# Kernel tuning notes

Hardware: AMD Instinct MI355X
Metric: run time of the kernel (lower is better)

## Reference

```python
import jax, jax.numpy as jnp
import numpy as np

EPS = 1e-5


def _conv(x, w, padding, groups=1):
    return jax.lax.conv_general_dilated(
        x, w, window_strides=(1, 1),
        padding=[(padding, padding), (padding, padding)],
        dimension_numbers=("NCHW", "OIHW", "NCHW"),
        feature_group_count=groups)


def _bn(x, gamma, beta, mean, var):
    # inference-mode BatchNorm2d, params shape [C]
    inv = gamma * jax.lax.rsqrt(var + EPS)
    return x * inv[None, :, None, None] + (beta - mean * inv)[None, :, None, None]


def _adder_dw(x, w):
    # depthwise AdderNet 'conv': out[b, c*R+r, h, w] = -sum_{kh,kw} |x[b,c,h+kh-p,w+kw-p] - w[c,r,kh,kw]|
    # x: [B,C,H,W], w: [C,R,K,K] (groups=C, R outputs per group)
    B, C, H, W = x.shape
    R, K = w.shape[1], w.shape[-1]
    p = K // 2
    xp = jnp.pad(x, ((0, 0), (0, 0), (p, p), (p, p)))
    acc = jnp.zeros((B, C, R, H, W), x.dtype)
    for kh in range(K):          # fixed small 3x3 tap loop
        for kw in range(K):
            shift = xp[:, :, kh:kh + H, kw:kw + W]          # [B,C,H,W]
            tap = w[:, :, kh, kw]                           # [C,R]
            acc = acc + jnp.abs(shift[:, :, None] - tap[None, :, :, None, None])
    return -acc.reshape(B, C * R, H, W)


def setup_inputs() -> dict:
    key = jax.random.key(0)
    ks = jax.random.split(key, 12)
    B, Cin, H, W = 32, 240, 56, 56
    init_c, ratio = 24, 10
    r1 = ratio - 1            # 9 ghost channels per primary channel
    new_c = init_c * r1       # 216
    f32 = jnp.float32
    x = jax.random.normal(ks[0], (B, Cin, H, W), f32)
    w_primary = jax.random.normal(ks[1], (init_c, Cin, 1, 1), f32) * 0.05
    w_dw = jax.random.normal(ks[2], (init_c, 1, 3, 3), f32) * 0.1
    w_add = jax.random.normal(ks[3], (init_c, r1, 3, 3), f32) * 0.1
    def bn(kk, c):
        k1, k2 = jax.random.split(kk)
        return (jnp.ones((c,), f32), jnp.zeros((c,), f32),
                jax.random.normal(k1, (c,), f32) * 0.1,
                jax.random.uniform(k2, (c,), f32, 0.5, 1.5))
    g1, b1, m1, v1 = bn(ks[4], init_c)
    g2, b2, m2, v2 = bn(ks[5], init_c)
    g3, b3, m3, v3 = bn(ks[6], new_c)
    return dict(x=x, w_primary=w_primary, g1=g1, b1=b1, m1=m1, v1=v1,
                w_dw=w_dw, g2=g2, b2=b2, m2=m2, v2=v2,
                w_add=w_add, g3=g3, b3=b3, m3=m3, v3=v3)


def reference(x, w_primary, g1, b1, m1, v1, w_dw, g2, b2, m2, v2,
              w_add, g3, b3, m3, v3):
    oup = 240
    init_c = w_primary.shape[0]
    # primary_conv: 1x1 conv -> BN -> depthwise 3x3 conv -> BN -> Identity (relu slot is Identity)
    x1 = _conv(x, w_primary, padding=0)
    x1 = _bn(x1, g1, b1, m1, v1)
    x1 = _conv(x1, w_dw, padding=1, groups=init_c)
    x1 = _bn(x1, g2, b2, m2, v2)
    # cheap_operation: depthwise Adder2D -> BN -> ReLU
    x2 = _adder_dw(x1, w_add)
    x2 = jax.nn.relu(_bn(x2, g3, b3, m3, v3))
    out = jnp.concatenate([x1, x2], axis=1)
    return out[:, :oup]
```

## Files before the change

kernel.cpp:

```cpp
#include <hip/hip_runtime.h>

#define EPS_ 1e-5f
#define BATCH 32
#define CIN 240
#define H_ 56
#define W_ 56
#define HW 3136
#define C1 24
#define R_ 9
#define C2 216
#define COUT 240

#define WS_WT   0
#define WS_B1   5760
#define WS_WDW  5784
#define WS_B2   6000
#define WS_INV3 6024
#define WS_T3   6240

__global__ __launch_bounds__(256) void prep_kernel(
    const float* __restrict__ wp,
    const float* __restrict__ g1, const float* __restrict__ b1,
    const float* __restrict__ m1, const float* __restrict__ v1,
    const float* __restrict__ wdw,
    const float* __restrict__ g2, const float* __restrict__ b2,
    const float* __restrict__ m2, const float* __restrict__ v2,
    const float* __restrict__ g3, const float* __restrict__ b3,
    const float* __restrict__ m3, const float* __restrict__ v3,
    float* __restrict__ ws) {
  int i = blockIdx.x * 256 + threadIdx.x;
  if (i < 5760) {
    int ci = i / C1, co = i % C1;
    float s = g1[co] / sqrtf(v1[co] + EPS_);
    ws[WS_WT + ci * C1 + co] = wp[co * CIN + ci] * s;
    if (ci == 0) ws[WS_B1 + co] = b1[co] - m1[co] * s;
  } else if (i < 5760 + C2) {
    int j = i - 5760;
    int c = j / 9;
    float s = g2[c] / sqrtf(v2[c] + EPS_);
    ws[WS_WDW + j] = wdw[j] * s;
    if (j % 9 == 0) ws[WS_B2 + c] = b2[c] - m2[c] * s;
  } else if (i < 5976 + C2) {
    int j = i - 5976;
    float s = g3[j] / sqrtf(v3[j] + EPS_);
    ws[WS_INV3 + j] = s;
    ws[WS_T3 + j] = b3[j] - m3[j] * s;
  }
}

__global__ __launch_bounds__(256) void conv1x1_kernel(
    const float* __restrict__ x, const float* __restrict__ wt,
    const float* __restrict__ bias1, float* __restrict__ out) {
  __shared__ float smem[6144];
  const int tid  = threadIdx.x;
  const int lane = tid & 63;
  const int kq   = tid >> 6;

  for (int i = tid; i < 5760; i += 256) smem[i] = wt[i];
  __syncthreads();

  const int P   = blockIdx.x * 64 + lane;
  const int b   = P / HW;
  const int hw  = P - b * HW;
  const int ci0 = kq * 60;
  const float* xp    = x + ((size_t)b * CIN + ci0) * HW + hw;
  const float* wbase = smem + ci0 * C1;

  float acc[C1];
#pragma unroll
  for (int i = 0; i < C1; ++i) acc[i] = 0.f;

  float A[6], B[6];
#pragma unroll
  for (int j = 0; j < 6; ++j) A[j] = xp[(size_t)j * HW];
#pragma unroll
  for (int j = 0; j < 6; ++j) B[j] = xp[(size_t)(6 + j) * HW];

  auto consume = [&](const float* buf, int cb) {
#pragma unroll
    for (int j = 0; j < 6; ++j) {
      const float xv = buf[j];
      const float* wr = wbase + (cb + j) * C1;
#pragma unroll
      for (int k = 0; k < 6; ++k) {
        const float4 wq = *(const float4*)(wr + 4 * k);
        acc[4*k+0] = fmaf(wq.x, xv, acc[4*k+0]);
        acc[4*k+1] = fmaf(wq.y, xv, acc[4*k+1]);
        acc[4*k+2] = fmaf(wq.z, xv, acc[4*k+2]);
        acc[4*k+3] = fmaf(wq.w, xv, acc[4*k+3]);
      }
    }
  };

#pragma unroll 1
  for (int g = 0; g < 4; ++g) {
    const int c = 12 * g;
    consume(A, c);
#pragma unroll
    for (int j = 0; j < 6; ++j) A[j] = xp[(size_t)(c + 12 + j) * HW];
    consume(B, c + 6);
#pragma unroll
    for (int j = 0; j < 6; ++j) B[j] = xp[(size_t)(c + 18 + j) * HW];
  }
  consume(A, 48);
  consume(B, 54);
  __syncthreads();

#pragma unroll
  for (int i = 0; i < C1; ++i) smem[(kq * C1 + i) * 64 + lane] = acc[i];
  __syncthreads();

  float* o = out + ((size_t)b * COUT + C1) * HW + hw;
#pragma unroll
  for (int i = 0; i < 6; ++i) {
    const int co = kq * 6 + i;
    float v = smem[(0 * C1 + co) * 64 + lane]
            + smem[(1 * C1 + co) * 64 + lane]
            + smem[(2 * C1 + co) * 64 + lane]
            + smem[(3 * C1 + co) * 64 + lane]
            + bias1[co];
    o[(size_t)co * HW] = v;
  }
}

__global__ __launch_bounds__(256) void dw_kernel(
    const float* __restrict__ outr, const float* __restrict__ wdwf,
    const float* __restrict__ bias2, float* __restrict__ out) {
  const int c = blockIdx.y, b = blockIdx.z;
  const int q = blockIdx.x * 256 + threadIdx.x;
  if (q >= 784) return;
  const int h  = q / 14;
  const int w0 = (q - h * 14) * 4;
  const float* in = outr + ((size_t)b * COUT + C1 + c) * HW;

  float wk[9];
#pragma unroll
  for (int k = 0; k < 9; ++k) wk[k] = wdwf[c * 9 + k];
  const float bb = bias2[c];

  float xr[3][6];
#pragma unroll
  for (int kh = 0; kh < 3; ++kh) {
    const int hh = h + kh - 1;
    const bool rok = (hh >= 0) & (hh < H_);
    const float* rp = in + hh * W_;
    xr[kh][0] = (rok && w0 > 0) ? rp[w0 - 1] : 0.f;
    if (rok) {
      const float4 m = *(const float4*)(rp + w0);
      xr[kh][1] = m.x; xr[kh][2] = m.y; xr[kh][3] = m.z; xr[kh][4] = m.w;
    } else {
      xr[kh][1] = 0.f; xr[kh][2] = 0.f; xr[kh][3] = 0.f; xr[kh][4] = 0.f;
    }
    xr[kh][5] = (rok && w0 < W_ - 4) ? rp[w0 + 4] : 0.f;
  }

  float4 v = {bb, bb, bb, bb};
#pragma unroll
  for (int kh = 0; kh < 3; ++kh) {
#pragma unroll
    for (int kw = 0; kw < 3; ++kw) {
      const float t = wk[kh * 3 + kw];
      v.x = fmaf(xr[kh][kw + 0], t, v.x);
      v.y = fmaf(xr[kh][kw + 1], t, v.y);
      v.z = fmaf(xr[kh][kw + 2], t, v.z);
      v.w = fmaf(xr[kh][kw + 3], t, v.w);
    }
  }
  *(float4*)(out + ((size_t)b * COUT + c) * HW + h * W_ + w0) = v;
}

__global__ __launch_bounds__(256) void adder_kernel(
    const float* __restrict__ outr, const float* __restrict__ wadd,
    const float* __restrict__ inv3, const float* __restrict__ t3,
    float* __restrict__ out) {
  const int c = blockIdx.y, b = blockIdx.z;
  __shared__ float taps[R_][3][4];
  __shared__ float s3[R_], t3s[R_];
  const int tid = threadIdx.x;
  if (tid < 108) {
    int r = tid / 12, kh = (tid / 4) % 3, kw = tid & 3;
    taps[r][kh][kw] = (kw < 3) ? wadd[((c * R_ + r) * 3 + kh) * 3 + kw] : 0.f;
  } else if (tid >= 128 && tid < 128 + R_) {
    int r = tid - 128;
    s3[r]  = inv3[c * R_ + r];
    t3s[r] = t3[c * R_ + r];
  }
  __syncthreads();

  const int q = blockIdx.x * 256 + tid;
  if (q >= 784) return;
  const int h  = q / 14;
  const int w0 = (q - h * 14) * 4;
  const float* in = outr + ((size_t)b * COUT + c) * HW;

  float xr[3][6];
#pragma unroll
  for (int kh = 0; kh < 3; ++kh) {
    const int hh = h + kh - 1;
    const bool rok = (hh >= 0) & (hh < H_);
    const float* rp = in + hh * W_;
    xr[kh][0] = (rok && w0 > 0) ? rp[w0 - 1] : 0.f;
    if (rok) {
      const float4 m = *(const float4*)(rp + w0);
      xr[kh][1] = m.x; xr[kh][2] = m.y; xr[kh][3] = m.z; xr[kh][4] = m.w;
    } else {
      xr[kh][1] = 0.f; xr[kh][2] = 0.f; xr[kh][3] = 0.f; xr[kh][4] = 0.f;
    }
    xr[kh][5] = (rok && w0 < W_ - 4) ? rp[w0 + 4] : 0.f;
  }

#pragma unroll
  for (int r = 0; r < R_; ++r) {
    float a0 = 0.f, a1 = 0.f, a2 = 0.f, a3 = 0.f;
#pragma unroll
    for (int kh = 0; kh < 3; ++kh) {
#pragma unroll
      for (int kw = 0; kw < 3; ++kw) {
        const float t = taps[r][kh][kw];
        a0 += fabsf(xr[kh][kw + 0] - t);
        a1 += fabsf(xr[kh][kw + 1] - t);
        a2 += fabsf(xr[kh][kw + 2] - t);
        a3 += fabsf(xr[kh][kw + 3] - t);
      }
    }
    const float s = s3[r], bb = t3s[r];
    float4 v;
    v.x = fmaxf(fmaf(-s, a0, bb), 0.f);
    v.y = fmaxf(fmaf(-s, a1, bb), 0.f);
    v.z = fmaxf(fmaf(-s, a2, bb), 0.f);
    v.w = fmaxf(fmaf(-s, a3, bb), 0.f);
    *(float4*)(out + ((size_t)b * COUT + C1 + c * R_ + r) * HW + h * W_ + w0) = v;
  }
}

extern "C" void kernel_launch(void* const* d_in, const int* in_sizes, int n_in,
                              void* d_out, int out_size, void* d_ws, size_t ws_size,
                              hipStream_t stream) {
  const float* x    = (const float*)d_in[0];
  const float* wp   = (const float*)d_in[1];
  const float* g1   = (const float*)d_in[2];
  const float* b1   = (const float*)d_in[3];
  const float* m1   = (const float*)d_in[4];
  const float* v1   = (const float*)d_in[5];
  const float* wdw  = (const float*)d_in[6];
  const float* g2   = (const float*)d_in[7];
  const float* b2   = (const float*)d_in[8];
  const float* m2   = (const float*)d_in[9];
  const float* v2   = (const float*)d_in[10];
  const float* wadd = (const float*)d_in[11];
  const float* g3   = (const float*)d_in[12];
  const float* b3   = (const float*)d_in[13];
  const float* m3   = (const float*)d_in[14];
  const float* v3   = (const float*)d_in[15];

  float* ws  = (float*)d_ws;
  float* out = (float*)d_out;

  prep_kernel<<<25, 256, 0, stream>>>(wp, g1, b1, m1, v1, wdw, g2, b2, m2, v2,
                                      g3, b3, m3, v3, ws);

  conv1x1_kernel<<<1568, 256, 0, stream>>>(x, ws + WS_WT, ws + WS_B1, out);

  dw_kernel<<<dim3(4, C1, BATCH), 256, 0, stream>>>(out, ws + WS_WDW,
                                                    ws + WS_B2, out);

  adder_kernel<<<dim3(4, C1, BATCH), 256, 0, stream>>>(out, wadd, ws + WS_INV3,
                                                       ws + WS_T3, out);
}
```

Measured before the change: 220.6 us.

## Fuse depthwise conv and adder into one tiled kernel; widen conv1x1 per thread

Fuses the depthwise 3x3 conv and the depthwise adder into one kernel. Each block stages a row tile of the 1x1 conv output in shared memory, computes the x1 tile with a halo, and then computes the nine adder outputs from shared memory. This removes one launch and the global round trip of x1. The 1x1 conv now computes two pixels per thread with float2 loads and writes into a workspace buffer, so it uses half as many blocks and twice the accumulator registers. A fallback to the old three-kernel path is used when the workspace is too small.

```diff
diff --git a/kernel.cpp b/kernel.cpp
--- a/kernel.cpp
+++ b/kernel.cpp
@@ -17,6 +17,8 @@
 #define WS_B2   6000
 #define WS_INV3 6024
 #define WS_T3   6240
+#define WS_T1   8192
+#define WS_T1_FLOATS (8192 + BATCH * C1 * HW)
 
 __global__ __launch_bounds__(256) void prep_kernel(
     const float* __restrict__ wp,
@@ -50,8 +52,9 @@
 
 __global__ __launch_bounds__(256) void conv1x1_kernel(
     const float* __restrict__ x, const float* __restrict__ wt,
-    const float* __restrict__ bias1, float* __restrict__ out) {
-  __shared__ float smem[6144];
+    const float* __restrict__ bias1, float* __restrict__ t1b,
+    const int cs, const int coff) {
+  __shared__ float smem[12288];
   const int tid  = threadIdx.x;
   const int lane = tid & 63;
   const int kq   = tid >> 6;
@@ -59,35 +62,39 @@
   for (int i = tid; i < 5760; i += 256) smem[i] = wt[i];
   __syncthreads();
 
-  const int P   = blockIdx.x * 64 + lane;
+  const int P   = blockIdx.x * 128 + lane * 2;
   const int b   = P / HW;
   const int hw  = P - b * HW;
   const int ci0 = kq * 60;
   const float* xp    = x + ((size_t)b * CIN + ci0) * HW + hw;
   const float* wbase = smem + ci0 * C1;
 
-  float acc[C1];
-#pragma unroll
-  for (int i = 0; i < C1; ++i) acc[i] = 0.f;
-
-  float A[6], B[6];
-#pragma unroll
-  for (int j = 0; j < 6; ++j) A[j] = xp[(size_t)j * HW];
-#pragma unroll
-  for (int j = 0; j < 6; ++j) B[j] = xp[(size_t)(6 + j) * HW];
-
-  auto consume = [&](const float* buf, int cb) {
+  float acc[C1][2];
+#pragma unroll
+  for (int i = 0; i < C1; ++i) { acc[i][0] = 0.f; acc[i][1] = 0.f; }
+
+  float2 A[6], B[6];
+#pragma unroll
+  for (int j = 0; j < 6; ++j) A[j] = *(const float2*)(xp + (size_t)j * HW);
+#pragma unroll
+  for (int j = 0; j < 6; ++j) B[j] = *(const float2*)(xp + (size_t)(6 + j) * HW);
+
+  auto consume = [&](const float2* buf, int cb) {
 #pragma unroll
     for (int j = 0; j < 6; ++j) {
-      const float xv = buf[j];
+      const float2 xv = buf[j];
       const float* wr = wbase + (cb + j) * C1;
 #pragma unroll
       for (int k = 0; k < 6; ++k) {
         const float4 wq = *(const float4*)(wr + 4 * k);
-        acc[4*k+0] = fmaf(wq.x, xv, acc[4*k+0]);
-        acc[4*k+1] = fmaf(wq.y, xv, acc[4*k+1]);
-        acc[4*k+2] = fmaf(wq.z, xv, acc[4*k+2]);
-        acc[4*k+3] = fmaf(wq.w, xv, acc[4*k+3]);
+        acc[4*k+0][0] = fmaf(wq.x, xv.x, acc[4*k+0][0]);
+        acc[4*k+0][1] = fmaf(wq.x, xv.y, acc[4*k+0][1]);
+        acc[4*k+1][0] = fmaf(wq.y, xv.x, acc[4*k+1][0]);
+        acc[4*k+1][1] = fmaf(wq.y, xv.y, acc[4*k+1][1]);
+        acc[4*k+2][0] = fmaf(wq.z, xv.x, acc[4*k+2][0]);
+        acc[4*k+2][1] = fmaf(wq.z, xv.y, acc[4*k+2][1]);
+        acc[4*k+3][0] = fmaf(wq.w, xv.x, acc[4*k+3][0]);
+        acc[4*k+3][1] = fmaf(wq.w, xv.y, acc[4*k+3][1]);
       }
     }
   };
@@ -97,31 +104,136 @@
     const int c = 12 * g;
     consume(A, c);
 #pragma unroll
-    for (int j = 0; j < 6; ++j) A[j] = xp[(size_t)(c + 12 + j) * HW];
+    for (int j = 0; j < 6; ++j) A[j] = *(const float2*)(xp + (size_t)(c + 12 + j) * HW);
     consume(B, c + 6);
 #pragma unroll
-    for (int j = 0; j < 6; ++j) B[j] = xp[(size_t)(c + 18 + j) * HW];
+    for (int j = 0; j < 6; ++j) B[j] = *(const float2*)(xp + (size_t)(c + 18 + j) * HW);
   }
   consume(A, 48);
   consume(B, 54);
   __syncthreads();
 
 #pragma unroll
-  for (int i = 0; i < C1; ++i) smem[(kq * C1 + i) * 64 + lane] = acc[i];
-  __syncthreads();
-
-  float* o = out + ((size_t)b * COUT + C1) * HW + hw;
+  for (int i = 0; i < C1; ++i)
+    *(float2*)&smem[(kq * C1 + i) * 128 + 2 * lane] = make_float2(acc[i][0], acc[i][1]);
+  __syncthreads();
+
+  float* o = t1b + ((size_t)b * cs + coff) * HW + hw;
 #pragma unroll
   for (int i = 0; i < 6; ++i) {
     const int co = kq * 6 + i;
-    float v = smem[(0 * C1 + co) * 64 + lane]
-            + smem[(1 * C1 + co) * 64 + lane]
-            + smem[(2 * C1 + co) * 64 + lane]
-            + smem[(3 * C1 + co) * 64 + lane]
-            + bias1[co];
-    o[(size_t)co * HW] = v;
-  }
-}
+    const float2 p0 = *(const float2*)&smem[(0 * C1 + co) * 128 + 2 * lane];
+    const float2 p1 = *(const float2*)&smem[(1 * C1 + co) * 128 + 2 * lane];
+    const float2 p2 = *(const float2*)&smem[(2 * C1 + co) * 128 + 2 * lane];
+    const float2 p3 = *(const float2*)&smem[(3 * C1 + co) * 128 + 2 * lane];
+    const float bsv = bias1[co];
+    float2 v;
+    v.x = p0.x + p1.x + p2.x + p3.x + bsv;
+    v.y = p0.y + p1.y + p2.y + p3.y + bsv;
+    *(float2*)(o + (size_t)co * HW) = v;
+  }
+}
+
+__global__ __launch_bounds__(256) void dwadd_kernel(
+    const float* __restrict__ t1b, const float* __restrict__ wdwf,
+    const float* __restrict__ bias2, const float* __restrict__ wadd,
+    const float* __restrict__ inv3, const float* __restrict__ t3,
+    float* __restrict__ out) {
+  const int c = blockIdx.y, b = blockIdx.z;
+  const int h0 = blockIdx.x * 14;
+  __shared__ __align__(16) float t1s[18 * 56];
+  __shared__ __align__(16) float x1s[16 * 56];
+  __shared__ float taps[R_][3][4];
+  __shared__ float s3[R_], t3s[R_];
+  const int tid = threadIdx.x;
+
+  const float* t1 = t1b + ((size_t)b * C1 + c) * HW;
+  if (tid < 252) {
+    const int r  = tid / 14;
+    const int w0 = (tid - r * 14) * 4;
+    const int gh = h0 - 2 + r;
+    float4 v = {0.f, 0.f, 0.f, 0.f};
+    if (gh >= 0 && gh < H_) v = *(const float4*)(t1 + gh * W_ + w0);
+    *(float4*)&t1s[r * 56 + w0] = v;
+  }
+  if (tid < 108) {
+    int r = tid / 12, kh = (tid / 4) % 3, kw = tid & 3;
+    taps[r][kh][kw] = (kw < 3) ? wadd[((c * R_ + r) * 3 + kh) * 3 + kw] : 0.f;
+  } else if (tid >= 128 && tid < 128 + R_) {
+    int r = tid - 128;
+    s3[r]  = inv3[c * R_ + r];
+    t3s[r] = t3[c * R_ + r];
+  }
+  float wk[9];
+#pragma unroll
+  for (int k = 0; k < 9; ++k) wk[k] = wdwf[c * 9 + k];
+  const float bb = bias2[c];
+  __syncthreads();
+
+  if (tid < 224) {
+    const int r  = tid / 14;
+    const int w0 = (tid - r * 14) * 4;
+    const int gr = h0 - 1 + r;
+    float4 v = {bb, bb, bb, bb};
+#pragma unroll
+    for (int kh = 0; kh < 3; ++kh) {
+      const float* rp = &t1s[(r + kh) * 56];
+      const float  l  = (w0 > 0) ? rp[w0 - 1] : 0.f;
+      const float4 m  = *(const float4*)(rp + w0);
+      const float  rt = (w0 < 52) ? rp[w0 + 4] : 0.f;
+      const float t0 = wk[kh * 3 + 0], t1w = wk[kh * 3 + 1], t2 = wk[kh * 3 + 2];
+      v.x = fmaf(l,   t0, v.x); v.x = fmaf(m.x, t1w, v.x); v.x = fmaf(m.y, t2, v.x);
+      v.y = fmaf(m.x, t0, v.y); v.y = fmaf(m.y, t1w, v.y); v.y = fmaf(m.z, t2, v.y);
+      v.z = fmaf(m.y, t0, v.z); v.z = fmaf(m.z, t1w, v.z); v.z = fmaf(m.w, t2, v.z);
+      v.w = fmaf(m.z, t0, v.w); v.w = fmaf(m.w, t1w, v.w); v.w = fmaf(rt,  t2, v.w);
+    }
+    float4 xv = v;
+    if (gr < 0 || gr >= H_) { xv.x = 0.f; xv.y = 0.f; xv.z = 0.f; xv.w = 0.f; }
+    *(float4*)&x1s[r * 56 + w0] = xv;
+    if (r >= 1 && r < 15)
+      *(float4*)(out + ((size_t)b * COUT + c) * HW + gr * W_ + w0) = v;
+  }
+  __syncthreads();
+
+  if (tid < 196) {
+    const int r  = tid / 14;
+    const int w0 = (tid - r * 14) * 4;
+    const int gr = h0 + r;
+    float xr[3][6];
+#pragma unroll
+    for (int kh = 0; kh < 3; ++kh) {
+      const float* rp = &x1s[(r + kh) * 56];
+      xr[kh][0] = (w0 > 0) ? rp[w0 - 1] : 0.f;
+      const float4 m = *(const float4*)(rp + w0);
+      xr[kh][1] = m.x; xr[kh][2] = m.y; xr[kh][3] = m.z; xr[kh][4] = m.w;
+      xr[kh][5] = (w0 < 52) ? rp[w0 + 4] : 0.f;
+    }
+    float* ob = out + ((size_t)b * COUT + C1 + c * R_) * HW + gr * W_ + w0;
+#pragma unroll
+    for (int rr = 0; rr < R_; ++rr) {
+      float a0 = 0.f, a1 = 0.f, a2 = 0.f, a3 = 0.f;
+#pragma unroll
+      for (int kh = 0; kh < 3; ++kh) {
+#pragma unroll
+        for (int kw = 0; kw < 3; ++kw) {
+          const float t = taps[rr][kh][kw];
+          a0 += fabsf(xr[kh][kw + 0] - t);
+          a1 += fabsf(xr[kh][kw + 1] - t);
+          a2 += fabsf(xr[kh][kw + 2] - t);
+          a3 += fabsf(xr[kh][kw + 3] - t);
+        }
+      }
+      const float s = s3[rr], tb = t3s[rr];
+      float4 v;
+      v.x = fmaxf(fmaf(-s, a0, tb), 0.f);
+      v.y = fmaxf(fmaf(-s, a1, tb), 0.f);
+      v.z = fmaxf(fmaf(-s, a2, tb), 0.f);
+      v.w = fmaxf(fmaf(-s, a3, tb), 0.f);
+      *(float4*)(ob + (size_t)rr * HW) = v;
+    }
+  }
+}
+
 
 __global__ __launch_bounds__(256) void dw_kernel(
     const float* __restrict__ outr, const float* __restrict__ wdwf,
@@ -256,14 +368,26 @@
   float* ws  = (float*)d_ws;
   float* out = (float*)d_out;
 
+  const bool fused = ws_size >= (size_t)WS_T1_FLOATS * sizeof(float);
+  float* t1b;
+  int cs, coff;
+  if (fused) { t1b = ws + WS_T1; cs = C1;   coff = 0; }
+  else       { t1b = out;        cs = COUT; coff = C1; }
+
   prep_kernel<<<25, 256, 0, stream>>>(wp, g1, b1, m1, v1, wdw, g2, b2, m2, v2,
                                       g3, b3, m3, v3, ws);
 
-  conv1x1_kernel<<<1568, 256, 0, stream>>>(x, ws + WS_WT, ws + WS_B1, out);
-
-  dw_kernel<<<dim3(4, C1, BATCH), 256, 0, stream>>>(out, ws + WS_WDW,
-                                                    ws + WS_B2, out);
-
-  adder_kernel<<<dim3(4, C1, BATCH), 256, 0, stream>>>(out, wadd, ws + WS_INV3,
-                                                       ws + WS_T3, out);
-}
+  conv1x1_kernel<<<784, 256, 0, stream>>>(x, ws + WS_WT, ws + WS_B1,
+                                          t1b, cs, coff);
+
+  if (fused) {
+    dwadd_kernel<<<dim3(4, C1, BATCH), 256, 0, stream>>>(
+        t1b, ws + WS_WDW, ws + WS_B2, wadd, ws + WS_INV3, ws + WS_T3, out);
+  } else {
+    dw_kernel<<<dim3(4, C1, BATCH), 256, 0, stream>>>(out, ws + WS_WDW,
+                                                      ws + WS_B2, out);
+    adder_kernel<<<dim3(4, C1, BATCH), 256, 0, stream>>>(out, wadd,
+                                                         ws + WS_INV3,
+                                                         ws + WS_T3, out);
+  }
+}
```

Result: no change. 219.1 us (-0.7%).
